# Optimization experiments

Hardware: AMD Instinct MI355X
Metric: run time of the kernel (lower is better)

The kernel has to match this reference:

```python
import jax, jax.numpy as jnp
import numpy as np

NBITS = 8
REDUCE = 64
OUT = 512


def setup_inputs() -> dict:
    key = jax.random.key(0)
    ks = jax.random.split(key, 6)
    T, B, C = 512, 16, 512
    ne = 2 ** NBITS
    x = jax.random.normal(ks[0], (T, B, C), dtype=jnp.float32)
    key_in = jax.random.normal(ks[1], (T, B, C), dtype=jnp.float32)  # unused by forward (overwritten)
    # xavier-ish init scales
    map_w = jax.random.normal(ks[2], (NBITS, C), dtype=jnp.float32) * np.sqrt(2.0 / (C + NBITS))
    map_b = jnp.zeros((NBITS,), dtype=jnp.float32)
    pw_w1 = jax.random.normal(ks[3], (REDUCE, C), dtype=jnp.float32) * np.sqrt(2.0 / (C + REDUCE))
    pw_w21 = jax.random.normal(ks[4], (ne, OUT * REDUCE), dtype=jnp.float32) * np.sqrt(2.0 / (ne + OUT * REDUCE))
    pw_w22 = jax.random.normal(ks[5], (ne, OUT * REDUCE), dtype=jnp.float32) * np.sqrt(2.0 / (ne + OUT * REDUCE))
    pw_B = jnp.zeros((1, 1, OUT), dtype=jnp.float32)
    return {"x": x, "key": key_in, "map_w": map_w, "map_b": map_b,
            "pw_w1": pw_w1, "pw_w21": pw_w21, "pw_w22": pw_w22, "pw_B": pw_B}


def reference(x, key, map_w, map_b, pw_w1, pw_w21, pw_w22, pw_B):
    # x: (T,B,C). `key` arg is overwritten by x in the original source.
    T, B, C = x.shape
    nbits = map_w.shape[0]
    out_dim = pw_B.shape[-1]
    reduce_dim = pw_w1.shape[0]

    k = x.reshape(T * B, C) @ map_w.T + map_b          # (T*B, nbits)
    z = jnp.clip(1.2 * jax.nn.sigmoid(k) - 0.1, 0.0, 1.0)  # saturated sigmoid
    code = (z > 0.5).astype(z.dtype)                   # eval: hard binary code

    pows = (2 ** jnp.arange(nbits, dtype=jnp.int32))   # bit_to_int weights
    qz1 = jnp.sum(code.astype(jnp.int32) * pows, axis=-1)          # (T*B,)
    qz2 = jnp.sum((1 - code.astype(jnp.int32)) * pows, axis=-1)    # (T*B,)

    # gather per-token expert rows and synthesize per-token weight matrix
    w2 = (pw_w21[qz1] + pw_w22[qz2]).reshape(T, B, out_dim, reduce_dim)

    # original computes (w2 @ pw_w1) @ x; reassociated as w2 @ (pw_w1 @ x)
    # to avoid materializing the (T,B,out,in) intermediate (same math)
    v = jnp.einsum('ri,tbi->tbr', pw_w1, x)            # (T,B,reduce)
    y = jnp.einsum('tbor,tbr->tbo', w2, v) + pw_B      # (T,B,out)

    loss = jnp.zeros((1,), dtype=x.dtype)
    return (y, loss)
```

## Files before the change

kernel.cpp:

```cpp
#include <hip/hip_runtime.h>

#define NTOK 8192
#define CDIM 512
#define NB   8
#define RD   64
#define OD   512
#define TPB_A 32
#define XPAD 4
#define XROW (CDIM + XPAD)

typedef unsigned char u8;

__global__ __launch_bounds__(256) void phaseA(
    const float* __restrict__ x, const float* __restrict__ map_w,
    const float* __restrict__ map_b, const float* __restrict__ w1,
    u8* __restrict__ q_out, float* __restrict__ v_out,
    float* __restrict__ loss_out)
{
    const int t    = threadIdx.x;
    const int tok0 = blockIdx.x * TPB_A;
    __shared__ float xs[TPB_A * XROW];

    const float4* xsrc = (const float4*)(x + (size_t)tok0 * CDIM);
    for (int i = t; i < TPB_A * (CDIM / 4); i += 256) {
        int r = i >> 7, c = i & 127;
        *((float4*)(xs + r * XROW) + c) = xsrc[i];
    }
    __syncthreads();

    {
        const int bit = t & 7, tk = t >> 3;
        const float4* m4 = (const float4*)(map_w + (size_t)bit * CDIM);
        const float4* x4 = (const float4*)(xs + tk * XROW);
        double a0 = 0.0, a1 = 0.0;
        for (int j = 0; j < CDIM / 4; ++j) {
            float4 m = m4[j], xv = x4[j];
            a0 += (double)m.x * (double)xv.x + (double)m.y * (double)xv.y;
            a1 += (double)m.z * (double)xv.z + (double)m.w * (double)xv.w;
        }
        double k = a0 + a1 + (double)map_b[bit];
        unsigned long long m = __ballot(k > 0.0);
        const int lane = t & 63;
        if ((lane & 7) == 0) {
            int g = lane >> 3;
            q_out[tok0 + tk] = (u8)((m >> (g * 8)) & 0xFFull);
        }
    }

    {
        const int r  = t & 63;
        const int tg = t >> 6;
        const float4* w4 = (const float4*)(w1 + (size_t)r * CDIM);
        float acc[8] = {0.f,0.f,0.f,0.f,0.f,0.f,0.f,0.f};
        for (int j = 0; j < CDIM / 4; ++j) {
            float4 wv = w4[j];
            #pragma unroll
            for (int k = 0; k < 8; ++k) {
                float4 xv = *((const float4*)(xs + (tg * 8 + k) * XROW) + j);
                acc[k] += wv.x * xv.x + wv.y * xv.y + wv.z * xv.z + wv.w * xv.w;
            }
        }
        #pragma unroll
        for (int k = 0; k < 8; ++k)
            v_out[(size_t)(tok0 + tg * 8 + k) * RD + r] = acc[k];
    }

    if (blockIdx.x == 0 && t == 0) loss_out[0] = 0.0f;
}

__global__ __launch_bounds__(512) void phaseB(
    const u8* __restrict__ q_arr, const float* __restrict__ v_arr,
    const float* __restrict__ w21, const float* __restrict__ w22,
    const float* __restrict__ pwB, float* __restrict__ y)
{
    const int q = blockIdx.x;
    const int t = threadIdx.x;
    __shared__ unsigned short list[NTOK];
    __shared__ int cnt;
    __shared__ float vs[8 * RD];

    if (t == 0) cnt = 0;
    __syncthreads();
    for (int i = t; i < NTOK; i += 512)
        if ((int)q_arr[i] == q) list[atomicAdd(&cnt, 1)] = (unsigned short)i;
    __syncthreads();
    const int n = cnt;
    if (n == 0) return;

    const float4* pa = (const float4*)(w21 + (size_t)q * (OD * RD) + (size_t)t * RD);
    const float4* pb = (const float4*)(w22 + (size_t)(255 - q) * (OD * RD) + (size_t)t * RD);
    float w[RD];
    #pragma unroll
    for (int j = 0; j < RD / 4; ++j) {
        float4 a = pa[j], b = pb[j];
        w[j * 4 + 0] = a.x + b.x;
        w[j * 4 + 1] = a.y + b.y;
        w[j * 4 + 2] = a.z + b.z;
        w[j * 4 + 3] = a.w + b.w;
    }
    const float bias = pwB[t];

    for (int base = 0; base < n; base += 8) {
        const int nb = min(8, n - base);
        if (t < nb * RD)
            vs[t] = v_arr[(size_t)list[base + (t >> 6)] * RD + (t & 63)];
        __syncthreads();
        for (int i = 0; i < nb; ++i) {
            float acc = bias;
            #pragma unroll
            for (int r = 0; r < RD; ++r) acc += w[r] * vs[i * RD + r];
            y[(size_t)list[base + i] * OD + t] = acc;
        }
        __syncthreads();
    }
}

__global__ __launch_bounds__(256) void mono(
    const float* __restrict__ x, const float* __restrict__ map_w,
    const float* __restrict__ map_b, const float* __restrict__ w1,
    const float* __restrict__ w21, const float* __restrict__ w22,
    const float* __restrict__ pwB, float* __restrict__ y)
{
    const int tok = blockIdx.x;
    const int t   = threadIdx.x;
    __shared__ float xsh[CDIM];
    __shared__ float vsh[RD];
    __shared__ int qsh;

    if (t == 0) qsh = 0;
    for (int i = t; i < CDIM; i += 256) xsh[i] = x[(size_t)tok * CDIM + i];
    __syncthreads();

    if (t < NB) {
        double a = 0.0;
        const float* mrow = map_w + (size_t)t * CDIM;
        for (int j = 0; j < CDIM; ++j) a += (double)mrow[j] * (double)xsh[j];
        a += (double)map_b[t];
        if (a > 0.0) atomicOr(&qsh, 1 << t);
    }
    if (t < RD) {
        const float* wrow = w1 + (size_t)t * CDIM;
        float acc = 0.f;
        for (int j = 0; j < CDIM; ++j) acc += wrow[j] * xsh[j];
        vsh[t] = acc;
    }
    __syncthreads();

    const int q = qsh;
    for (int o = t; o < OD; o += 256) {
        const float* pa = w21 + (size_t)q * (OD * RD) + (size_t)o * RD;
        const float* pb = w22 + (size_t)(255 - q) * (OD * RD) + (size_t)o * RD;
        float acc = pwB[o];
        for (int r = 0; r < RD; ++r) acc += (pa[r] + pb[r]) * vsh[r];
        y[(size_t)tok * OD + o] = acc;
    }
    if (tok == 0 && t == 0) y[(size_t)NTOK * OD] = 0.0f;
}

extern "C" void kernel_launch(void* const* d_in, const int* in_sizes, int n_in,
                              void* d_out, int out_size, void* d_ws, size_t ws_size,
                              hipStream_t stream) {
    const float* x     = (const float*)d_in[0];
    const float* map_w = (const float*)d_in[2];
    const float* map_b = (const float*)d_in[3];
    const float* w1    = (const float*)d_in[4];
    const float* w21   = (const float*)d_in[5];
    const float* w22   = (const float*)d_in[6];
    const float* pwB   = (const float*)d_in[7];
    float* out = (float*)d_out;

    const size_t need = (size_t)NTOK + (size_t)NTOK * RD * sizeof(float);
    if (ws_size >= need) {
        u8*    q_ws = (u8*)d_ws;
        float* v_ws = (float*)((char*)d_ws + NTOK);
        phaseA<<<NTOK / TPB_A, 256, 0, stream>>>(x, map_w, map_b, w1, q_ws, v_ws,
                                                 out + (size_t)NTOK * OD);
        phaseB<<<256, 512, 0, stream>>>(q_ws, v_ws, w21, w22, pwB, out);
    } else {
        mono<<<NTOK, 256, 0, stream>>>(x, map_w, map_b, w1, w21, w22, pwB, out);
    }
}
```

Before: 201.8 us.

## Split expert blocks four ways and shrink phaseA tiles for more parallelism

PhaseA now handles 8 tokens per 128-thread block, splitting each code-bit dot product across two lanes combined by a shuffle, and computes 4 tokens per thread for the v projection. PhaseB launches four 128-thread blocks per expert, each covering a quarter of the outputs. Each block issues its expert weight loads before the token scan, reads the code array with 16-byte loads, and processes two tokens per inner step. The aim is to fill more compute units and overlap weight fetches with list building, at the cost of every block rescanning the full code array.

```diff
diff --git a/kernel.cpp b/kernel.cpp
--- a/kernel.cpp
+++ b/kernel.cpp
@@ -5,13 +5,19 @@
 #define NB   8
 #define RD   64
 #define OD   512
-#define TPB_A 32
-#define XPAD 4
-#define XROW (CDIM + XPAD)
+
+#define TPB_A 8
+#define XPAD  4
+#define XROW  (CDIM + XPAD)
+#define XROW4 (XROW / 4)
 
 typedef unsigned char u8;
 
-__global__ __launch_bounds__(256) void phaseA(
+__device__ __forceinline__ float4 f4add(float4 a, float4 b) {
+    return make_float4(a.x + b.x, a.y + b.y, a.z + b.z, a.w + b.w);
+}
+
+__global__ __launch_bounds__(128) void phaseA(
     const float* __restrict__ x, const float* __restrict__ map_w,
     const float* __restrict__ map_b, const float* __restrict__ w1,
     u8* __restrict__ q_out, float* __restrict__ v_out,
@@ -19,31 +25,35 @@
 {
     const int t    = threadIdx.x;
     const int tok0 = blockIdx.x * TPB_A;
-    __shared__ float xs[TPB_A * XROW];
+    __shared__ __align__(16) float xs[TPB_A * XROW];
 
     const float4* xsrc = (const float4*)(x + (size_t)tok0 * CDIM);
-    for (int i = t; i < TPB_A * (CDIM / 4); i += 256) {
+    #pragma unroll
+    for (int i = t; i < TPB_A * (CDIM / 4); i += 128) {
         int r = i >> 7, c = i & 127;
         *((float4*)(xs + r * XROW) + c) = xsrc[i];
     }
     __syncthreads();
 
     {
-        const int bit = t & 7, tk = t >> 3;
-        const float4* m4 = (const float4*)(map_w + (size_t)bit * CDIM);
-        const float4* x4 = (const float4*)(xs + tk * XROW);
+        const int bit  = t & 7;
+        const int half = (t >> 3) & 1;
+        const int tk   = t >> 4;
+        const float4* m4 = (const float4*)(map_w + (size_t)bit * CDIM) + half * 64;
+        const float4* x4 = (const float4*)xs + tk * XROW4 + half * 64;
         double a0 = 0.0, a1 = 0.0;
-        for (int j = 0; j < CDIM / 4; ++j) {
+        for (int j = 0; j < 64; ++j) {
             float4 m = m4[j], xv = x4[j];
             a0 += (double)m.x * (double)xv.x + (double)m.y * (double)xv.y;
             a1 += (double)m.z * (double)xv.z + (double)m.w * (double)xv.w;
         }
-        double k = a0 + a1 + (double)map_b[bit];
-        unsigned long long m = __ballot(k > 0.0);
-        const int lane = t & 63;
-        if ((lane & 7) == 0) {
-            int g = lane >> 3;
-            q_out[tok0 + tk] = (u8)((m >> (g * 8)) & 0xFFull);
+        double a = a0 + a1;
+        a += __shfl_xor(a, 8);
+        const double k = a + (double)map_b[bit];
+        const unsigned long long m = __ballot(k > 0.0);
+        if ((t & 15) == 0) {
+            int g = (t >> 4) & 3;
+            q_out[tok0 + tk] = (u8)((m >> (g * 16)) & 0xFFull);
         }
     }
 
@@ -51,65 +61,109 @@
         const int r  = t & 63;
         const int tg = t >> 6;
         const float4* w4 = (const float4*)(w1 + (size_t)r * CDIM);
-        float acc[8] = {0.f,0.f,0.f,0.f,0.f,0.f,0.f,0.f};
+        const float4* xb = (const float4*)xs + (size_t)(tg * 4) * XROW4;
+        float acc0 = 0.f, acc1 = 0.f, acc2 = 0.f, acc3 = 0.f;
         for (int j = 0; j < CDIM / 4; ++j) {
             float4 wv = w4[j];
-            #pragma unroll
-            for (int k = 0; k < 8; ++k) {
-                float4 xv = *((const float4*)(xs + (tg * 8 + k) * XROW) + j);
-                acc[k] += wv.x * xv.x + wv.y * xv.y + wv.z * xv.z + wv.w * xv.w;
-            }
-        }
-        #pragma unroll
-        for (int k = 0; k < 8; ++k)
-            v_out[(size_t)(tok0 + tg * 8 + k) * RD + r] = acc[k];
+            float4 x0 = xb[j];
+            float4 x1 = xb[XROW4 + j];
+            float4 x2 = xb[2 * XROW4 + j];
+            float4 x3 = xb[3 * XROW4 + j];
+            acc0 += wv.x * x0.x + wv.y * x0.y + wv.z * x0.z + wv.w * x0.w;
+            acc1 += wv.x * x1.x + wv.y * x1.y + wv.z * x1.z + wv.w * x1.w;
+            acc2 += wv.x * x2.x + wv.y * x2.y + wv.z * x2.z + wv.w * x2.w;
+            acc3 += wv.x * x3.x + wv.y * x3.y + wv.z * x3.z + wv.w * x3.w;
+        }
+        float* vo = v_out + (size_t)(tok0 + tg * 4) * RD + r;
+        vo[0 * RD] = acc0; vo[1 * RD] = acc1; vo[2 * RD] = acc2; vo[3 * RD] = acc3;
     }
 
     if (blockIdx.x == 0 && t == 0) loss_out[0] = 0.0f;
 }
 
-__global__ __launch_bounds__(512) void phaseB(
+__global__ __launch_bounds__(128) void phaseB(
     const u8* __restrict__ q_arr, const float* __restrict__ v_arr,
     const float* __restrict__ w21, const float* __restrict__ w22,
     const float* __restrict__ pwB, float* __restrict__ y)
 {
-    const int q = blockIdx.x;
-    const int t = threadIdx.x;
+    const int q  = blockIdx.x >> 2;
+    const int qu = blockIdx.x & 3;
+    const int t  = threadIdx.x;
+    const int o  = qu * 128 + t;
+
     __shared__ unsigned short list[NTOK];
     __shared__ int cnt;
-    __shared__ float vs[8 * RD];
+    __shared__ __align__(16) float vs[8 * RD];
+
+    const float4* pa = (const float4*)w21 + (size_t)q * (OD * RD / 4) + (size_t)o * (RD / 4);
+    const float4* pb = (const float4*)w22 + (size_t)(255 - q) * (OD * RD / 4) + (size_t)o * (RD / 4);
+    float4 a0 = pa[0],  a1 = pa[1],  a2 = pa[2],  a3 = pa[3],
+           a4 = pa[4],  a5 = pa[5],  a6 = pa[6],  a7 = pa[7],
+           a8 = pa[8],  a9 = pa[9],  a10 = pa[10], a11 = pa[11],
+           a12 = pa[12], a13 = pa[13], a14 = pa[14], a15 = pa[15];
+    float4 b0 = pb[0],  b1 = pb[1],  b2 = pb[2],  b3 = pb[3],
+           b4 = pb[4],  b5 = pb[5],  b6 = pb[6],  b7 = pb[7],
+           b8 = pb[8],  b9 = pb[9],  b10 = pb[10], b11 = pb[11],
+           b12 = pb[12], b13 = pb[13], b14 = pb[14], b15 = pb[15];
 
     if (t == 0) cnt = 0;
     __syncthreads();
-    for (int i = t; i < NTOK; i += 512)
-        if ((int)q_arr[i] == q) list[atomicAdd(&cnt, 1)] = (unsigned short)i;
+
+    const uint4* qa = (const uint4*)q_arr;
+    for (int i = t; i < NTOK / 16; i += 128) {
+        uint4 u = qa[i];
+        int sbase = i * 16;
+#define CHK(WORD, OFF) { unsigned uw = (WORD); \
+        if ((int)(uw & 0xFFu)         == q) list[atomicAdd(&cnt, 1)] = (unsigned short)(sbase + (OFF));     \
+        if ((int)((uw >> 8)  & 0xFFu) == q) list[atomicAdd(&cnt, 1)] = (unsigned short)(sbase + (OFF) + 1); \
+        if ((int)((uw >> 16) & 0xFFu) == q) list[atomicAdd(&cnt, 1)] = (unsigned short)(sbase + (OFF) + 2); \
+        if ((int)(uw >> 24)           == q) list[atomicAdd(&cnt, 1)] = (unsigned short)(sbase + (OFF) + 3); }
+        CHK(u.x, 0) CHK(u.y, 4) CHK(u.z, 8) CHK(u.w, 12)
+#undef CHK
+    }
     __syncthreads();
     const int n = cnt;
     if (n == 0) return;
 
-    const float4* pa = (const float4*)(w21 + (size_t)q * (OD * RD) + (size_t)t * RD);
-    const float4* pb = (const float4*)(w22 + (size_t)(255 - q) * (OD * RD) + (size_t)t * RD);
-    float w[RD];
-    #pragma unroll
-    for (int j = 0; j < RD / 4; ++j) {
-        float4 a = pa[j], b = pb[j];
-        w[j * 4 + 0] = a.x + b.x;
-        w[j * 4 + 1] = a.y + b.y;
-        w[j * 4 + 2] = a.z + b.z;
-        w[j * 4 + 3] = a.w + b.w;
-    }
-    const float bias = pwB[t];
-
+    float4 w0 = f4add(a0, b0),  w1 = f4add(a1, b1),  w2 = f4add(a2, b2),  w3 = f4add(a3, b3),
+           w4 = f4add(a4, b4),  w5 = f4add(a5, b5),  w6 = f4add(a6, b6),  w7 = f4add(a7, b7),
+           w8 = f4add(a8, b8),  w9 = f4add(a9, b9),  w10 = f4add(a10, b10), w11 = f4add(a11, b11),
+           w12 = f4add(a12, b12), w13 = f4add(a13, b13), w14 = f4add(a14, b14), w15 = f4add(a15, b15);
+    const float bias = pwB[o];
+
+    const float4* v4 = (const float4*)v_arr;
     for (int base = 0; base < n; base += 8) {
         const int nb = min(8, n - base);
-        if (t < nb * RD)
-            vs[t] = v_arr[(size_t)list[base + (t >> 6)] * RD + (t & 63)];
+        if (t < nb * 16)
+            ((float4*)vs)[t] = v4[(size_t)list[base + (t >> 4)] * (RD / 4) + (t & 15)];
         __syncthreads();
-        for (int i = 0; i < nb; ++i) {
-            float acc = bias;
-            #pragma unroll
-            for (int r = 0; r < RD; ++r) acc += w[r] * vs[i * RD + r];
-            y[(size_t)list[base + i] * OD + t] = acc;
+        int i = 0;
+        for (; i + 2 <= nb; i += 2) {
+            const float4* p0 = (const float4*)vs + (size_t)i * 16;
+            const float4* p1 = p0 + 16;
+            float acc0 = bias, acc1 = bias;
+#define STEP(J, W) { float4 u0 = p0[J], u1 = p1[J]; \
+            acc0 += W.x * u0.x + W.y * u0.y + W.z * u0.z + W.w * u0.w; \
+            acc1 += W.x * u1.x + W.y * u1.y + W.z * u1.z + W.w * u1.w; }
+            STEP(0, w0)  STEP(1, w1)  STEP(2, w2)  STEP(3, w3)
+            STEP(4, w4)  STEP(5, w5)  STEP(6, w6)  STEP(7, w7)
+            STEP(8, w8)  STEP(9, w9)  STEP(10, w10) STEP(11, w11)
+            STEP(12, w12) STEP(13, w13) STEP(14, w14) STEP(15, w15)
+#undef STEP
+            y[(size_t)list[base + i]     * OD + o] = acc0;
+            y[(size_t)list[base + i + 1] * OD + o] = acc1;
+        }
+        if (i < nb) {
+            const float4* p0 = (const float4*)vs + (size_t)i * 16;
+            float acc0 = bias;
+#define STEP1(J, W) { float4 u0 = p0[J]; \
+            acc0 += W.x * u0.x + W.y * u0.y + W.z * u0.z + W.w * u0.w; }
+            STEP1(0, w0)  STEP1(1, w1)  STEP1(2, w2)  STEP1(3, w3)
+            STEP1(4, w4)  STEP1(5, w5)  STEP1(6, w6)  STEP1(7, w7)
+            STEP1(8, w8)  STEP1(9, w9)  STEP1(10, w10) STEP1(11, w11)
+            STEP1(12, w12) STEP1(13, w13) STEP1(14, w14) STEP1(15, w15)
+#undef STEP1
+            y[(size_t)list[base + i] * OD + o] = acc0;
         }
         __syncthreads();
     }
@@ -173,9 +227,9 @@
     if (ws_size >= need) {
         u8*    q_ws = (u8*)d_ws;
         float* v_ws = (float*)((char*)d_ws + NTOK);
-        phaseA<<<NTOK / TPB_A, 256, 0, stream>>>(x, map_w, map_b, w1, q_ws, v_ws,
+        phaseA<<<NTOK / TPB_A, 128, 0, stream>>>(x, map_w, map_b, w1, q_ws, v_ws,
                                                  out + (size_t)NTOK * OD);
-        phaseB<<<256, 512, 0, stream>>>(q_ws, v_ws, w21, w22, pwB, out);
+        phaseB<<<256 * 4, 128, 0, stream>>>(q_ws, v_ws, w21, w22, pwB, out);
     } else {
         mono<<<NTOK, 256, 0, stream>>>(x, map_w, map_b, w1, w21, w22, pwB, out);
     }
```

Result: no change. 198.5 us (-1.6%).
